# Performance work log

Measured on AMD Instinct MI355X. Metric: run time of the kernel, lower is better.

Reference implementation:

```python
import jax, jax.numpy as jnp
import numpy as np

INPUT_DIM = 2048
DIM = 1024
CODEBOOK_SIZE = 8192
COMMITMENT_COST = 0.25
N = 8192


def setup_inputs() -> dict:
    key = jax.random.key(0)
    ks = jax.random.split(key, 6)
    s_in = 1.0 / np.sqrt(INPUT_DIM)
    s_d = 1.0 / np.sqrt(DIM)
    return {
        "roi_feats": jax.random.normal(ks[0], (N, INPUT_DIM), dtype=jnp.float32),
        "W_in": jax.random.normal(ks[1], (DIM, INPUT_DIM), dtype=jnp.float32) * s_in,
        "b_in": jnp.zeros((DIM,), dtype=jnp.float32),
        "W_enc": jax.random.normal(ks[2], (DIM, DIM), dtype=jnp.float32) * s_d,
        "b_enc": jnp.zeros((DIM,), dtype=jnp.float32),
        "codebook": jax.random.uniform(ks[3], (CODEBOOK_SIZE, DIM), dtype=jnp.float32,
                                        minval=-1.0 / CODEBOOK_SIZE, maxval=1.0 / CODEBOOK_SIZE),
        "W_dec": jax.random.normal(ks[4], (DIM, DIM), dtype=jnp.float32) * s_d,
        "b_dec": jnp.zeros((DIM,), dtype=jnp.float32),
        "W_out": jax.random.normal(ks[5], (INPUT_DIM, DIM), dtype=jnp.float32) * s_d,
        "b_out": jnp.zeros((INPUT_DIM,), dtype=jnp.float32),
    }


def reference(roi_feats, W_in, b_in, W_enc, b_enc, codebook, W_dec, b_dec, W_out, b_out):
    # encoder(input_projection(x))
    z_e = (roi_feats @ W_in.T + b_in) @ W_enc.T + b_enc  # [N, DIM]
    # squared-euclidean distances to codebook: [N, K]
    d = (jnp.sum(z_e * z_e, axis=1, keepdims=True)
         - 2.0 * (z_e @ codebook.T)
         + jnp.sum(codebook * codebook, axis=1))
    ids = jnp.argmin(d, axis=-1)  # [N]
    z_q_raw = codebook[ids]  # [N, DIM]
    # straight-through estimator
    z_q = z_e + jax.lax.stop_gradient(z_q_raw - z_e)
    recon = (z_q @ W_dec.T + b_dec) @ W_out.T + b_out  # [N, INPUT_DIM]
    recon_loss = jnp.mean((recon - roi_feats) ** 2)
    embedding_loss = jnp.mean((jax.lax.stop_gradient(z_q) - z_e) ** 2)
    commitment_loss = jnp.mean((z_q - jax.lax.stop_gradient(z_e)) ** 2)
    vq_loss = recon_loss + embedding_loss + COMMITMENT_COST * commitment_loss
    return ids, z_q, recon, vq_loss, recon_loss, embedding_loss, commitment_loss
```

## Files before the change

### kernel.cpp

```cpp
#include <hip/hip_runtime.h>
#include <float.h>


#define N_ROWS 8192
#define IN_DIM 2048
#define DIM 1024
#define CBK 8192

#define PANEL_MASK_K1024_C32 0x0000000000401000ULL
#define PANEL_MASK_K2048_C32 0x0101001001001000ULL

#define SCREEN_DELTA 1.2e-3f

typedef __attribute__((ext_vector_type(8))) short short8;
typedef __attribute__((ext_vector_type(8))) unsigned short ushort8;
typedef __attribute__((ext_vector_type(4))) float f32x4;

__device__ __forceinline__ float sqf(float v) { return __builtin_fmaf(v, v, 0.0f); }

__device__ __forceinline__ unsigned short f2bf(float f) {
  unsigned int u = __float_as_uint(f);
  u += 0x7fffu + ((u >> 16) & 1u);
  return (unsigned short)(u >> 16);
}

__device__ __forceinline__ int swz128(int c) {
  return (c & 3) | (((c >> 3) & 7) << 2) | (((c >> 2) & 1) << 5) | ((c >> 6) << 6);
}

__device__ __forceinline__ float block_reduce_sum(float v) {
  __shared__ float sh[4];
  #pragma unroll
  for (int off = 32; off > 0; off >>= 1) v += __shfl_down(v, off, 64);
  const int lane = threadIdx.x & 63, w = threadIdx.x >> 6;
  if (lane == 0) sh[w] = v;
  __syncthreads();
  float r = 0.f;
  if (threadIdx.x == 0) r = sh[0] + sh[1] + sh[2] + sh[3];
  return r;
}

__device__ __forceinline__ float chain_d(const float* __restrict__ zsh,
                                         const float* __restrict__ cbr,
                                         float z2r, float c2e) {
  float part = 0.f;
  for (int k = 0; k < 384; ++k) part = __builtin_fmaf(zsh[k], cbr[k], part);
  float total = part;
  part = 0.f;
  for (int k = 384; k < 704; ++k) part = __builtin_fmaf(zsh[k], cbr[k], part);
  total = total + part;
  part = 0.f;
  for (int k = 704; k < 1024; ++k) part = __builtin_fmaf(zsh[k], cbr[k], part);
  total = total + part;
  return __builtin_fmaf(-2.0f, total, z2r) + c2e;
}

template <bool BT>
__global__ __launch_bounds__(256) void gemm128(
    const float* __restrict__ A, const float* __restrict__ B,
    const float* __restrict__ bias, float* __restrict__ C,
    int M, int N, int K) {
  __shared__ float As[2][16][132];
  __shared__ float Bs[2][16][132];
  const int tid = threadIdx.x;
  const int tx = tid & 15, ty = tid >> 4;
  const int bm = blockIdx.y, bn = blockIdx.x;

  const int mload = tid & 127, kh = tid >> 7;
  const size_t arow = (size_t)(bm * 128 + mload) * (size_t)K;
  const size_t brow = BT ? (size_t)(bn * 128 + mload) * (size_t)K : 0;
  const int swn = swz128(mload);
  const int c4 = (tid & 31) << 2;
  const int kr = tid >> 5;
  const int swc = swz128(c4);

  float acc[8][8];
  #pragma unroll
  for (int r = 0; r < 8; ++r)
    #pragma unroll
    for (int c = 0; c < 8; ++c) acc[r][c] = 0.f;

  const int boff = ((tx & 7) << 2) | ((tx >> 3) << 6);

  float4 av0, av1, bv0, bv1;
  av0 = *(const float4*)&A[arow + kh * 8];
  av1 = *(const float4*)&A[arow + kh * 8 + 4];
  if (BT) {
    bv0 = *(const float4*)&B[brow + kh * 8];
    bv1 = *(const float4*)&B[brow + kh * 8 + 4];
  } else {
    bv0 = *(const float4*)&B[(size_t)kr * N + bn * 128 + c4];
    bv1 = *(const float4*)&B[(size_t)(kr + 8) * N + bn * 128 + c4];
  }
  As[0][kh * 8 + 0][mload] = av0.x; As[0][kh * 8 + 1][mload] = av0.y;
  As[0][kh * 8 + 2][mload] = av0.z; As[0][kh * 8 + 3][mload] = av0.w;
  As[0][kh * 8 + 4][mload] = av1.x; As[0][kh * 8 + 5][mload] = av1.y;
  As[0][kh * 8 + 6][mload] = av1.z; As[0][kh * 8 + 7][mload] = av1.w;
  if (BT) {
    Bs[0][kh * 8 + 0][swn] = bv0.x; Bs[0][kh * 8 + 1][swn] = bv0.y;
    Bs[0][kh * 8 + 2][swn] = bv0.z; Bs[0][kh * 8 + 3][swn] = bv0.w;
    Bs[0][kh * 8 + 4][swn] = bv1.x; Bs[0][kh * 8 + 5][swn] = bv1.y;
    Bs[0][kh * 8 + 6][swn] = bv1.z; Bs[0][kh * 8 + 7][swn] = bv1.w;
  } else {
    *(float4*)&Bs[0][kr][swc] = bv0;
    *(float4*)&Bs[0][kr + 8][swc] = bv1;
  }
  const int nk = K >> 4;
  if (nk > 1) {
    av0 = *(const float4*)&A[arow + 16 + kh * 8];
    av1 = *(const float4*)&A[arow + 16 + kh * 8 + 4];
    if (BT) {
      bv0 = *(const float4*)&B[brow + 16 + kh * 8];
      bv1 = *(const float4*)&B[brow + 16 + kh * 8 + 4];
    } else {
      bv0 = *(const float4*)&B[(size_t)(16 + kr) * N + bn * 128 + c4];
      bv1 = *(const float4*)&B[(size_t)(16 + kr + 8) * N + bn * 128 + c4];
    }
  }
  __syncthreads();

  for (int ki = 0; ki < nk; ++ki) {
    const int p = ki & 1;
    if (ki + 1 < nk) {
      As[p ^ 1][kh * 8 + 0][mload] = av0.x; As[p ^ 1][kh * 8 + 1][mload] = av0.y;
      As[p ^ 1][kh * 8 + 2][mload] = av0.z; As[p ^ 1][kh * 8 + 3][mload] = av0.w;
      As[p ^ 1][kh * 8 + 4][mload] = av1.x; As[p ^ 1][kh * 8 + 5][mload] = av1.y;
      As[p ^ 1][kh * 8 + 6][mload] = av1.z; As[p ^ 1][kh * 8 + 7][mload] = av1.w;
      if (BT) {
        Bs[p ^ 1][kh * 8 + 0][swn] = bv0.x; Bs[p ^ 1][kh * 8 + 1][swn] = bv0.y;
        Bs[p ^ 1][kh * 8 + 2][swn] = bv0.z; Bs[p ^ 1][kh * 8 + 3][swn] = bv0.w;
        Bs[p ^ 1][kh * 8 + 4][swn] = bv1.x; Bs[p ^ 1][kh * 8 + 5][swn] = bv1.y;
        Bs[p ^ 1][kh * 8 + 6][swn] = bv1.z; Bs[p ^ 1][kh * 8 + 7][swn] = bv1.w;
      } else {
        *(float4*)&Bs[p ^ 1][kr][swc] = bv0;
        *(float4*)&Bs[p ^ 1][kr + 8][swc] = bv1;
      }
      if (ki + 2 < nk) {
        const int k2 = (ki + 2) << 4;
        av0 = *(const float4*)&A[arow + k2 + kh * 8];
        av1 = *(const float4*)&A[arow + k2 + kh * 8 + 4];
        if (BT) {
          bv0 = *(const float4*)&B[brow + k2 + kh * 8];
          bv1 = *(const float4*)&B[brow + k2 + kh * 8 + 4];
        } else {
          bv0 = *(const float4*)&B[(size_t)(k2 + kr) * N + bn * 128 + c4];
          bv1 = *(const float4*)&B[(size_t)(k2 + kr + 8) * N + bn * 128 + c4];
        }
      }
    }
    #pragma unroll
    for (int kk = 0; kk < 16; ++kk) {
      const float4 a0 = *(const float4*)&As[p][kk][ty * 8];
      const float4 a1 = *(const float4*)&As[p][kk][ty * 8 + 4];
      const float4 b0 = *(const float4*)&Bs[p][kk][boff];
      const float4 b1 = *(const float4*)&Bs[p][kk][boff + 32];
      const float ar[8] = {a0.x, a0.y, a0.z, a0.w, a1.x, a1.y, a1.z, a1.w};
      const float br[8] = {b0.x, b0.y, b0.z, b0.w, b1.x, b1.y, b1.z, b1.w};
      #pragma unroll
      for (int r = 0; r < 8; ++r)
        #pragma unroll
        for (int c = 0; c < 8; ++c) acc[r][c] = fmaf(ar[r], br[c], acc[r][c]);
    }
    __syncthreads();
  }

  const int gcol = bn * 128 + tx * 8;
  float bb[8] = {0, 0, 0, 0, 0, 0, 0, 0};
  if (bias) {
    const float4 v0 = *(const float4*)&bias[gcol];
    const float4 v1 = *(const float4*)&bias[gcol + 4];
    bb[0] = v0.x; bb[1] = v0.y; bb[2] = v0.z; bb[3] = v0.w;
    bb[4] = v1.x; bb[5] = v1.y; bb[6] = v1.z; bb[7] = v1.w;
  }
  #pragma unroll
  for (int r = 0; r < 8; ++r) {
    float* cp = &C[(size_t)(bm * 128 + ty * 8 + r) * N + gcol];
    float4 o0, o1;
    o0.x = acc[r][0] + bb[0]; o0.y = acc[r][1] + bb[1];
    o0.z = acc[r][2] + bb[2]; o0.w = acc[r][3] + bb[3];
    o1.x = acc[r][4] + bb[4]; o1.y = acc[r][5] + bb[5];
    o1.z = acc[r][6] + bb[6]; o1.w = acc[r][7] + bb[7];
    *(float4*)cp = o0;
    *(float4*)(cp + 4) = o1;
  }
}

__global__ __launch_bounds__(256) void emul_gemm_kernel(
    const float* __restrict__ A, const float* __restrict__ B,
    const float* __restrict__ bias, float* __restrict__ C,
    int N, int K, int lda, int ldb, unsigned long long panel_mask) {
  __shared__ float As_[2][32][128];
  __shared__ float Bs_[2][32][128];
  const int tid = threadIdx.x;
  const int tx = tid & 15, ty = tid >> 4;
  const int row0 = blockIdx.y * 128, col0 = blockIdx.x * 128;
  const int sr = tid & 127, sh = tid >> 7;
  const int scol = (((sr >> 2) & 1) << 6) + ((sr >> 3) << 2) + (sr & 3);

  float part[8][8], total[8][8];
  #pragma unroll
  for (int r = 0; r < 8; ++r)
    #pragma unroll
    for (int e = 0; e < 8; ++e) { part[r][e] = 0.f; total[r][e] = 0.f; }

  float4 av[4], bv[4];
  #pragma unroll
  for (int q = 0; q < 4; ++q) {
    av[q] = *(const float4*)&A[(size_t)(row0 + sr) * lda + sh * 16 + q * 4];
    bv[q] = *(const float4*)&B[(size_t)(col0 + sr) * ldb + sh * 16 + q * 4];
  }
  #pragma unroll
  for (int q = 0; q < 4; ++q) {
    As_[0][sh * 16 + q * 4 + 0][sr] = av[q].x;
    As_[0][sh * 16 + q * 4 + 1][sr] = av[q].y;
    As_[0][sh * 16 + q * 4 + 2][sr] = av[q].z;
    As_[0][sh * 16 + q * 4 + 3][sr] = av[q].w;
    Bs_[0][sh * 16 + q * 4 + 0][scol] = bv[q].x;
    Bs_[0][sh * 16 + q * 4 + 1][scol] = bv[q].y;
    Bs_[0][sh * 16 + q * 4 + 2][scol] = bv[q].z;
    Bs_[0][sh * 16 + q * 4 + 3][scol] = bv[q].w;
  }
  const int nch = K >> 5;
  if (nch > 1) {
    #pragma unroll
    for (int q = 0; q < 4; ++q) {
      av[q] = *(const float4*)&A[(size_t)(row0 + sr) * lda + 32 + sh * 16 + q * 4];
      bv[q] = *(const float4*)&B[(size_t)(col0 + sr) * ldb + 32 + sh * 16 + q * 4];
    }
  }
  __syncthreads();

  for (int ci = 0; ci < nch; ++ci) {
    const int p = ci & 1;
    if (ci + 1 < nch) {
      #pragma unroll
      for (int q = 0; q < 4; ++q) {
        As_[p ^ 1][sh * 16 + q * 4 + 0][sr] = av[q].x;
        As_[p ^ 1][sh * 16 + q * 4 + 1][sr] = av[q].y;
        As_[p ^ 1][sh * 16 + q * 4 + 2][sr] = av[q].z;
        As_[p ^ 1][sh * 16 + q * 4 + 3][sr] = av[q].w;
        Bs_[p ^ 1][sh * 16 + q * 4 + 0][scol] = bv[q].x;
        Bs_[p ^ 1][sh * 16 + q * 4 + 1][scol] = bv[q].y;
        Bs_[p ^ 1][sh * 16 + q * 4 + 2][scol] = bv[q].z;
        Bs_[p ^ 1][sh * 16 + q * 4 + 3][scol] = bv[q].w;
      }
      if (ci + 2 < nch) {
        const int k2 = (ci + 2) << 5;
        #pragma unroll
        for (int q = 0; q < 4; ++q) {
          av[q] = *(const float4*)&A[(size_t)(row0 + sr) * lda + k2 + sh * 16 + q * 4];
          bv[q] = *(const float4*)&B[(size_t)(col0 + sr) * ldb + k2 + sh * 16 + q * 4];
        }
      }
    }
    if (ci && ((panel_mask >> ci) & 1ULL)) {
      #pragma unroll
      for (int r = 0; r < 8; ++r)
        #pragma unroll
        for (int e = 0; e < 8; ++e) { total[r][e] = total[r][e] + part[r][e]; part[r][e] = 0.f; }
    }
    #pragma unroll 4
    for (int kk = 0; kk < 32; ++kk) {
      const float4 za = *(const float4*)&As_[p][kk][ty * 8];
      const float4 zb = *(const float4*)&As_[p][kk][ty * 8 + 4];
      const float4 ca = *(const float4*)&Bs_[p][kk][tx * 4];
      const float4 cb4 = *(const float4*)&Bs_[p][kk][64 + tx * 4];
      const float zr[8] = {za.x, za.y, za.z, za.w, zb.x, zb.y, zb.z, zb.w};
      const float cr[8] = {ca.x, ca.y, ca.z, ca.w, cb4.x, cb4.y, cb4.z, cb4.w};
      #pragma unroll
      for (int r = 0; r < 8; ++r)
        #pragma unroll
        for (int e = 0; e < 8; ++e)
          part[r][e] = __builtin_fmaf(zr[r], cr[e], part[r][e]);
    }
    __syncthreads();
  }
  #pragma unroll
  for (int r = 0; r < 8; ++r)
    #pragma unroll
    for (int e = 0; e < 8; ++e) total[r][e] = total[r][e] + part[r][e];

  const float4 ba = *(const float4*)&bias[col0 + tx * 8];
  const float4 bb = *(const float4*)&bias[col0 + tx * 8 + 4];
  const float br8[8] = {ba.x, ba.y, ba.z, ba.w, bb.x, bb.y, bb.z, bb.w};
  #pragma unroll
  for (int r = 0; r < 8; ++r) {
    float* cp = &C[(size_t)(row0 + ty * 8 + r) * N + col0 + tx * 8];
    float4 o0, o1;
    o0.x = total[r][0] + br8[0]; o0.y = total[r][1] + br8[1];
    o0.z = total[r][2] + br8[2]; o0.w = total[r][3] + br8[3];
    o1.x = total[r][4] + br8[4]; o1.y = total[r][5] + br8[5];
    o1.z = total[r][6] + br8[6]; o1.w = total[r][7] + br8[7];
    *(float4*)cp = o0;
    *(float4*)(cp + 4) = o1;
  }
}

__global__ __launch_bounds__(256) void zsplit_kernel(
    const float* __restrict__ Z, unsigned* __restrict__ ZP) {
  const size_t base = (size_t)blockIdx.x * 1024 + threadIdx.x * 4;
  const float4 v = *(const float4*)&Z[base];
  const float xf[4] = {v.x, v.y, v.z, v.w};
  uint4 o;
  unsigned ov[4];
  #pragma unroll
  for (int i = 0; i < 4; ++i) {
    const unsigned u = __float_as_uint(xf[i]);
    const unsigned hb = u & 0xFFFF0000u;
    const float rem = xf[i] - __uint_as_float(hb);
    ov[i] = (u >> 16) | (__float_as_uint(rem) & 0xFFFF0000u);
  }
  o.x = ov[0]; o.y = ov[1]; o.z = ov[2]; o.w = ov[3];
  *(uint4*)&ZP[base] = o;
}

__global__ __launch_bounds__(256) void mfma_screen_kernel(
    const unsigned* __restrict__ ZP, const float* __restrict__ CB,
    const float* __restrict__ Z2, const float* __restrict__ C2,
    uint4* __restrict__ recs) {
  __shared__ unsigned short Zs[128 * 64];
  __shared__ unsigned short Cs[128 * 64];
  __shared__ int rowminI[128];
  __shared__ int cnt[128];
  __shared__ unsigned short cand[128][12];
  const int tid = threadIdx.x;
  const int wid = tid >> 6, lane = tid & 63;
  const int e0 = blockIdx.x * 128, row0 = blockIdx.y * 128;
  const int wr = (wid >> 1) * 64, wc = (wid & 1) * 64;

  if (tid < 128) { rowminI[tid] = 0x7F800000; cnt[tid] = 0; }

  f32x4 acc[4][4];
  #pragma unroll
  for (int m = 0; m < 4; ++m)
    #pragma unroll
    for (int n = 0; n < 4; ++n)
      #pragma unroll
      for (int j = 0; j < 4; ++j) acc[m][n][j] = 0.f;

  const int stg_r = tid >> 3, stg_kg = (tid & 7) * 4;

  for (int k0 = 0; k0 < 1024; k0 += 32) {
    __syncthreads();
    #pragma unroll
    for (int s = 0; s < 4; ++s) {
      const int r = stg_r + s * 32;
      const int swz = (r & 7) << 4;
      const int bhi = (r * 128 + stg_kg * 2) ^ swz;
      const int blo = (r * 128 + 64 + stg_kg * 2) ^ swz;
      const uint4 p = *(const uint4*)&ZP[(size_t)(row0 + r) * 1024 + k0 + stg_kg];
      uint2 zh, zl;
      zh.x = (p.x & 0xFFFFu) | (p.y << 16);
      zh.y = (p.z & 0xFFFFu) | (p.w << 16);
      zl.x = (p.x >> 16) | (p.y & 0xFFFF0000u);
      zl.y = (p.z >> 16) | (p.w & 0xFFFF0000u);
      *(uint2*)((char*)Zs + bhi) = zh;
      *(uint2*)((char*)Zs + blo) = zl;
      const float4 cv = *(const float4*)&CB[(size_t)(e0 + r) * 1024 + k0 + stg_kg];
      const float cf[4] = {cv.x, cv.y, cv.z, cv.w};
      unsigned ch[4], cl[4];
      #pragma unroll
      for (int i = 0; i < 4; ++i) {
        const unsigned u = __float_as_uint(cf[i]);
        ch[i] = u & 0xFFFF0000u;
        const float rem = cf[i] - __uint_as_float(ch[i]);
        cl[i] = __float_as_uint(rem) & 0xFFFF0000u;
      }
      uint2 cph, cpl;
      cph.x = (ch[0] >> 16) | ch[1];
      cph.y = (ch[2] >> 16) | ch[3];
      cpl.x = (cl[0] >> 16) | cl[1];
      cpl.y = (cl[2] >> 16) | cl[3];
      *(uint2*)((char*)Cs + bhi) = cph;
      *(uint2*)((char*)Cs + blo) = cpl;
    }
    __syncthreads();
    const int kb2 = 16 * (lane >> 4);
    short8 ah[4], al[4], bh[4], bl[4];
    #pragma unroll
    for (int m = 0; m < 4; ++m) {
      const int r = wr + m * 16 + (lane & 15);
      const int swz = (r & 7) << 4;
      ah[m] = *(const short8*)((const char*)Zs + ((r * 128 + kb2) ^ swz));
      al[m] = *(const short8*)((const char*)Zs + ((r * 128 + 64 + kb2) ^ swz));
    }
    #pragma unroll
    for (int n = 0; n < 4; ++n) {
      const int r = wc + n * 16 + (lane & 15);
      const int swz = (r & 7) << 4;
      bh[n] = *(const short8*)((const char*)Cs + ((r * 128 + kb2) ^ swz));
      bl[n] = *(const short8*)((const char*)Cs + ((r * 128 + 64 + kb2) ^ swz));
    }
    #pragma unroll
    for (int m = 0; m < 4; ++m)
      #pragma unroll
      for (int n = 0; n < 4; ++n) {
        acc[m][n] = __builtin_amdgcn_mfma_f32_16x16x32_bf16(ah[m], bh[n], acc[m][n], 0, 0, 0);
        acc[m][n] = __builtin_amdgcn_mfma_f32_16x16x32_bf16(ah[m], bl[n], acc[m][n], 0, 0, 0);
        acc[m][n] = __builtin_amdgcn_mfma_f32_16x16x32_bf16(al[m], bh[n], acc[m][n], 0, 0, 0);
      }
  }

  float dv[4][4][4];
  #pragma unroll
  for (int m = 0; m < 4; ++m)
    #pragma unroll
    for (int j = 0; j < 4; ++j) {
      const int rg = row0 + wr + m * 16 + (lane >> 4) * 4 + j;
      const float z2r = Z2[rg];
      float lm = FLT_MAX;
      #pragma unroll
      for (int n = 0; n < 4; ++n) {
        const float d = __builtin_fmaf(-2.0f, acc[m][n][j], z2r) +
                        C2[e0 + wc + n * 16 + (lane & 15)];
        dv[m][n][j] = d;
        lm = fminf(lm, d);
      }
      atomicMin(&rowminI[wr + m * 16 + (lane >> 4) * 4 + j], __float_as_int(lm));
    }
  __syncthreads();
  #pragma unroll
  for (int m = 0; m < 4; ++m)
    #pragma unroll
    for (int j = 0; j < 4; ++j) {
      const int rl = wr + m * 16 + (lane >> 4) * 4 + j;
      const float thr = __int_as_float(rowminI[rl]) + SCREEN_DELTA;
      #pragma unroll
      for (int n = 0; n < 4; ++n) {
        if (dv[m][n][j] <= thr) {
          const int pos = atomicAdd(&cnt[rl], 1);
          if (pos < 12)
            cand[rl][pos] = (unsigned short)(e0 + wc + n * 16 + (lane & 15));
        }
      }
    }
  __syncthreads();
  if (tid < 128) {
    uint4 a, b;
    a.x = (unsigned)rowminI[tid];
    a.y = (unsigned)cnt[tid];
    a.z = (unsigned)cand[tid][0] | ((unsigned)cand[tid][1] << 16);
    a.w = (unsigned)cand[tid][2] | ((unsigned)cand[tid][3] << 16);
    b.x = (unsigned)cand[tid][4] | ((unsigned)cand[tid][5] << 16);
    b.y = (unsigned)cand[tid][6] | ((unsigned)cand[tid][7] << 16);
    b.z = (unsigned)cand[tid][8] | ((unsigned)cand[tid][9] << 16);
    b.w = (unsigned)cand[tid][10] | ((unsigned)cand[tid][11] << 16);
    const size_t base = ((size_t)(row0 + tid) * 64 + blockIdx.x) * 2;
    recs[base] = a;
    recs[base + 1] = b;
  }
}

__global__ __launch_bounds__(256) void collect_rescore_kernel(
    const uint4* __restrict__ recs, const float* __restrict__ Z,
    const float* __restrict__ CB, const float* __restrict__ Z2,
    const float* __restrict__ C2, int* __restrict__ ids,
    float* __restrict__ o_ids) {
  __shared__ float zsh[1024];
  __shared__ float gmin_sh;
  __shared__ int lcnt, ovf;
  __shared__ unsigned short list[64];
  __shared__ unsigned long long kred[4];
  const int row = blockIdx.x, tid = threadIdx.x;
  if (tid == 0) { lcnt = 0; ovf = 0; }
  uint4 r0 = make_uint4(0, 0, 0, 0), r1 = make_uint4(0, 0, 0, 0);
  float mymin = FLT_MAX;
  if (tid < 64) {
    const size_t base = ((size_t)row * 64 + tid) * 2;
    r0 = recs[base];
    r1 = recs[base + 1];
    mymin = __uint_as_float(r0.x);
  }
  for (int i = tid; i < 1024; i += 256) zsh[i] = Z[(size_t)row * 1024 + i];
  if (tid < 64) {
    float m = mymin;
    #pragma unroll
    for (int off = 32; off > 0; off >>= 1) m = fminf(m, __shfl_down(m, off, 64));
    if (tid == 0) gmin_sh = m;
  }
  __syncthreads();
  const float thr = gmin_sh + SCREEN_DELTA;
  if (tid < 64 && mymin <= thr) {
    const int c = (int)r0.y;
    if (c > 12) {
      atomicOr(&ovf, 1);
    } else {
      unsigned short idxs[12];
      idxs[0] = r0.z & 0xFFFF; idxs[1] = r0.z >> 16;
      idxs[2] = r0.w & 0xFFFF; idxs[3] = r0.w >> 16;
      idxs[4] = r1.x & 0xFFFF; idxs[5] = r1.x >> 16;
      idxs[6] = r1.y & 0xFFFF; idxs[7] = r1.y >> 16;
      idxs[8] = r1.z & 0xFFFF; idxs[9] = r1.z >> 16;
      idxs[10] = r1.w & 0xFFFF; idxs[11] = r1.w >> 16;
      for (int i = 0; i < c; ++i) {
        const int pos = atomicAdd(&lcnt, 1);
        if (pos < 64) list[pos] = idxs[i];
        else atomicOr(&ovf, 1);
      }
    }
  }
  __syncthreads();
  const float z2r = Z2[row];
  unsigned long long key = ~0ULL;
  if (ovf) {
    for (int e = tid; e < CBK; e += 256) {
      const float d = chain_d(zsh, &CB[(size_t)e * 1024], z2r, C2[e]);
      const unsigned long long k =
          ((unsigned long long)__float_as_uint(d) << 32) | (unsigned)e;
      key = (k < key) ? k : key;
    }
  } else {
    const int n = lcnt < 64 ? lcnt : 64;
    if (tid < n) {
      const int e = list[tid];
      const float d = chain_d(zsh, &CB[(size_t)e * 1024], z2r, C2[e]);
      key = ((unsigned long long)__float_as_uint(d) << 32) | (unsigned)e;
    }
  }
  #pragma unroll
  for (int off = 32; off > 0; off >>= 1) {
    const unsigned long long o = __shfl_down(key, off, 64);
    key = (o < key) ? o : key;
  }
  if ((tid & 63) == 0) kred[tid >> 6] = key;
  __syncthreads();
  if (tid == 0) {
    unsigned long long k = kred[0];
    k = (kred[1] < k) ? kred[1] : k;
    k = (kred[2] < k) ? kred[2] : k;
    k = (kred[3] < k) ? kred[3] : k;
    const int e = (int)(k & 0xFFFFFFFFu);
    ids[row] = e;
    o_ids[row] = (float)e;
  }
}

__global__ __launch_bounds__(256) void mfma_recon_kernel(
    const float* __restrict__ A, const float* __restrict__ B,
    const float* __restrict__ bias, float* __restrict__ C) {
  __shared__ unsigned short Abf[128 * 64];
  __shared__ unsigned short Bbf[128 * 64];
  const int tid = threadIdx.x;
  const int wid = tid >> 6, lane = tid & 63;
  const int row0 = blockIdx.y * 128, col0 = blockIdx.x * 128;
  const int wr = (wid >> 1) * 64, wc = (wid & 1) * 64;

  f32x4 acc[4][4];
  #pragma unroll
  for (int m = 0; m < 4; ++m)
    #pragma unroll
    for (int n = 0; n < 4; ++n)
      #pragma unroll
      for (int j = 0; j < 4; ++j) acc[m][n][j] = 0.f;

  for (int k0 = 0; k0 < 1024; k0 += 64) {
    __syncthreads();
    #pragma unroll
    for (int q = 0; q < 4; ++q) {
      const int g = tid + q * 256;
      const int r = g >> 3;
      const int kg = (g & 7) * 8;
      const float4 a0 = *(const float4*)&A[(size_t)(row0 + r) * 1024 + k0 + kg];
      const float4 a1 = *(const float4*)&A[(size_t)(row0 + r) * 1024 + k0 + kg + 4];
      const float4 b0 = *(const float4*)&B[(size_t)(col0 + r) * 1024 + k0 + kg];
      const float4 b1 = *(const float4*)&B[(size_t)(col0 + r) * 1024 + k0 + kg + 4];
      ushort8 pa, pb;
      pa[0] = f2bf(a0.x); pa[1] = f2bf(a0.y); pa[2] = f2bf(a0.z); pa[3] = f2bf(a0.w);
      pa[4] = f2bf(a1.x); pa[5] = f2bf(a1.y); pa[6] = f2bf(a1.z); pa[7] = f2bf(a1.w);
      pb[0] = f2bf(b0.x); pb[1] = f2bf(b0.y); pb[2] = f2bf(b0.z); pb[3] = f2bf(b0.w);
      pb[4] = f2bf(b1.x); pb[5] = f2bf(b1.y); pb[6] = f2bf(b1.z); pb[7] = f2bf(b1.w);
      const int byte = (r * 128 + kg * 2) ^ ((r & 7) << 4);
      *(ushort8*)((char*)Abf + byte) = pa;
      *(ushort8*)((char*)Bbf + byte) = pb;
    }
    __syncthreads();
    #pragma unroll
    for (int kh = 0; kh < 2; ++kh) {
      const int kb = kh * 32 + 8 * (lane >> 4);
      short8 afr[4], bfr[4];
      #pragma unroll
      for (int m = 0; m < 4; ++m) {
        const int r = wr + m * 16 + (lane & 15);
        const int byte = (r * 128 + kb * 2) ^ ((r & 7) << 4);
        afr[m] = *(const short8*)((const char*)Abf + byte);
      }
      #pragma unroll
      for (int n = 0; n < 4; ++n) {
        const int r = wc + n * 16 + (lane & 15);
        const int byte = (r * 128 + kb * 2) ^ ((r & 7) << 4);
        bfr[n] = *(const short8*)((const char*)Bbf + byte);
      }
      #pragma unroll
      for (int m = 0; m < 4; ++m)
        #pragma unroll
        for (int n = 0; n < 4; ++n)
          acc[m][n] = __builtin_amdgcn_mfma_f32_16x16x32_bf16(
              afr[m], bfr[n], acc[m][n], 0, 0, 0);
    }
  }

  #pragma unroll
  for (int m = 0; m < 4; ++m)
    #pragma unroll
    for (int n = 0; n < 4; ++n) {
      const int col = col0 + wc + n * 16 + (lane & 15);
      const float bc = bias[col];
      #pragma unroll
      for (int j = 0; j < 4; ++j) {
        const int row = row0 + wr + m * 16 + (lane >> 4) * 4 + j;
        C[(size_t)row * 2048 + col] = acc[m][n][j] + bc;
      }
    }
}

__global__ __launch_bounds__(256) void sumsq1024_kernel(
    const float* __restrict__ X, float* __restrict__ out) {
  __shared__ float rows[4][1024];
  __shared__ float leaves[4][8];
  const int tid = threadIdx.x;
  const int row0 = blockIdx.x * 4;
  for (int i = tid; i < 4096; i += 256)
    rows[i >> 10][i & 1023] = X[(size_t)row0 * 1024 + i];
  __syncthreads();
  if (tid < 32) {
    const int r = tid >> 3, lf = tid & 7;
    const float* a = &rows[r][lf * 128];
    float s0 = sqf(a[0]), s1 = sqf(a[1]), s2 = sqf(a[2]), s3 = sqf(a[3]);
    float s4 = sqf(a[4]), s5 = sqf(a[5]), s6 = sqf(a[6]), s7 = sqf(a[7]);
    for (int i = 8; i < 128; i += 8) {
      s0 = s0 + sqf(a[i + 0]); s1 = s1 + sqf(a[i + 1]);
      s2 = s2 + sqf(a[i + 2]); s3 = s3 + sqf(a[i + 3]);
      s4 = s4 + sqf(a[i + 4]); s5 = s5 + sqf(a[i + 5]);
      s6 = s6 + sqf(a[i + 6]); s7 = s7 + sqf(a[i + 7]);
    }
    leaves[r][lf] = ((s0 + s1) + (s2 + s3)) + ((s4 + s5) + (s6 + s7));
  }
  __syncthreads();
  if (tid < 4) {
    const float* L = leaves[tid];
    const float p01 = L[0] + L[1], p23 = L[2] + L[3];
    const float p45 = L[4] + L[5], p67 = L[6] + L[7];
    out[row0 + tid] = ((p01 + p23) + (p45 + p67));
  }
}

__global__ __launch_bounds__(256) void gather_zq_kernel(
    const float* __restrict__ cb, const int* __restrict__ ids,
    float* __restrict__ zq) {
  const int row = blockIdx.x;
  const int id = ids[row];
  const float4 v = *(const float4*)&cb[(size_t)id * DIM + threadIdx.x * 4];
  *(float4*)&zq[(size_t)row * DIM + threadIdx.x * 4] = v;
}

__global__ __launch_bounds__(256) void rowdot_bias_kernel(
    const float* __restrict__ W, const float* __restrict__ v,
    const float* __restrict__ b2, float* __restrict__ out) {
  const int row = blockIdx.x;
  const float4 w4 = *(const float4*)&W[(size_t)row * 1024 + threadIdx.x * 4];
  const float4 v4 = *(const float4*)&v[threadIdx.x * 4];
  const float s = w4.x * v4.x + w4.y * v4.y + w4.z * v4.z + w4.w * v4.w;
  const float r = block_reduce_sum(s);
  if (threadIdx.x == 0) out[row] = r + b2[row];
}

__global__ __launch_bounds__(256) void sqdiff_partial_kernel(
    const float* __restrict__ a, const float* __restrict__ b,
    float* __restrict__ part) {
  const size_t base = (size_t)blockIdx.x * 2048 + (size_t)threadIdx.x * 8;
  const float4 x0 = *(const float4*)&a[base];
  const float4 x1 = *(const float4*)&a[base + 4];
  const float4 y0 = *(const float4*)&b[base];
  const float4 y1 = *(const float4*)&b[base + 4];
  float s = 0.f;
  float d;
  d = x0.x - y0.x; s += d * d; d = x0.y - y0.y; s += d * d;
  d = x0.z - y0.z; s += d * d; d = x0.w - y0.w; s += d * d;
  d = x1.x - y1.x; s += d * d; d = x1.y - y1.y; s += d * d;
  d = x1.z - y1.z; s += d * d; d = x1.w - y1.w; s += d * d;
  const float r = block_reduce_sum(s);
  if (threadIdx.x == 0) part[blockIdx.x] = r;
}

__global__ __launch_bounds__(256) void final_losses_kernel(
    const float* __restrict__ rp, const float* __restrict__ ep,
    float* __restrict__ o) {
  __shared__ double sh[4];
  const int lane = threadIdx.x & 63, w = threadIdx.x >> 6;
  double s = 0.0;
  for (int i = threadIdx.x; i < 8192; i += 256) s += (double)rp[i];
  #pragma unroll
  for (int off = 32; off > 0; off >>= 1) s += __shfl_down(s, off, 64);
  if (lane == 0) sh[w] = s;
  __syncthreads();
  double rl = 0.0;
  if (threadIdx.x == 0) rl = (sh[0] + sh[1] + sh[2] + sh[3]) / ((double)N_ROWS * IN_DIM);
  __syncthreads();
  double s2 = 0.0;
  for (int i = threadIdx.x; i < 4096; i += 256) s2 += (double)ep[i];
  #pragma unroll
  for (int off = 32; off > 0; off >>= 1) s2 += __shfl_down(s2, off, 64);
  if (lane == 0) sh[w] = s2;
  __syncthreads();
  if (threadIdx.x == 0) {
    const double el = (sh[0] + sh[1] + sh[2] + sh[3]) / ((double)N_ROWS * DIM);
    o[0] = (float)(rl + el + 0.25 * el);
    o[1] = (float)rl;
    o[2] = (float)el;
    o[3] = (float)el;
  }
}

extern "C" void kernel_launch(void* const* d_in, const int* in_sizes, int n_in,
                              void* d_out, int out_size, void* d_ws, size_t ws_size,
                              hipStream_t stream) {
  const float* roi   = (const float*)d_in[0];
  const float* W_in  = (const float*)d_in[1];
  const float* b_in  = (const float*)d_in[2];
  const float* W_enc = (const float*)d_in[3];
  const float* b_enc = (const float*)d_in[4];
  const float* cb    = (const float*)d_in[5];
  const float* W_dec = (const float*)d_in[6];
  const float* b_dec = (const float*)d_in[7];
  const float* W_out = (const float*)d_in[8];
  const float* b_out = (const float*)d_in[9];

  float* out = (float*)d_out;
  float* o_ids   = out;
  float* o_zq    = out + 8192;
  float* o_recon = out + 8192 + (size_t)N_ROWS * DIM;
  float* o_scal  = out + 8192 + (size_t)N_ROWS * DIM + (size_t)N_ROWS * IN_DIM;

  float*  ws    = (float*)d_ws;
  float*  W_dc  = ws;
  float*  z2    = ws + 2097152;
  float*  c2    = ws + 2105344;
  int*    ids   = (int*)(ws + 2113536);
  float*  b_dc  = ws + 2121728;
  float*  ep    = ws + 2123776;
  float*  rp    = ws + 2127872;

  float*    t     = o_recon;
  float*    z     = o_recon + (size_t)N_ROWS * DIM;
  unsigned* zpack = (unsigned*)o_recon;
  uint4*    recs  = (uint4*)o_zq;

  rowdot_bias_kernel<<<IN_DIM, 256, 0, stream>>>(W_out, b_dec, b_out, b_dc);
  gemm128<false><<<dim3(DIM / 128, IN_DIM / 128), 256, 0, stream>>>(
      W_out, W_dec, nullptr, W_dc, IN_DIM, DIM, DIM);

  emul_gemm_kernel<<<dim3(DIM / 128, N_ROWS / 128), 256, 0, stream>>>(
      roi, W_in, b_in, t, DIM, IN_DIM, IN_DIM, IN_DIM, PANEL_MASK_K2048_C32);
  emul_gemm_kernel<<<dim3(DIM / 128, N_ROWS / 128), 256, 0, stream>>>(
      t, W_enc, b_enc, z, DIM, DIM, DIM, DIM, PANEL_MASK_K1024_C32);

  sumsq1024_kernel<<<N_ROWS / 4, 256, 0, stream>>>(z, z2);
  sumsq1024_kernel<<<CBK / 4, 256, 0, stream>>>(cb, c2);

  zsplit_kernel<<<N_ROWS, 256, 0, stream>>>(z, zpack);

  mfma_screen_kernel<<<dim3(CBK / 128, N_ROWS / 128), 256, 0, stream>>>(
      zpack, cb, z2, c2, recs);
  collect_rescore_kernel<<<N_ROWS, 256, 0, stream>>>(
      recs, z, cb, z2, c2, ids, o_ids);

  gather_zq_kernel<<<N_ROWS, 256, 0, stream>>>(cb, ids, o_zq);
  sqdiff_partial_kernel<<<(N_ROWS * DIM) / 2048, 256, 0, stream>>>(o_zq, z, ep);

  mfma_recon_kernel<<<dim3(IN_DIM / 128, N_ROWS / 128), 256, 0, stream>>>(
      o_zq, W_dc, b_dc, o_recon);

  sqdiff_partial_kernel<<<(N_ROWS * IN_DIM) / 2048, 256, 0, stream>>>(
      o_recon, roi, rp);
  final_losses_kernel<<<1, 256, 0, stream>>>(rp, ep, o_scal);
}
```

Baseline: 1.486 ms.

## Fuse z split, zq gather and embedding loss; widen screen K tile

The bf16 hi/lo split of z moves into the epilogue of the second encoder GEMM, and the codebook gather plus per-row embedding-loss sum move into the rescoring kernel. This removes the separate zsplit, gather and sqdiff kernels and their extra passes over memory. The screening kernel now stages 64 K-elements per iteration with twice the shared memory, halving barrier count. Its row-min atomics are reduced across 16 lanes by shuffles first. Workspace aliasing of recs and zpack is swapped between the output buffers, and the larger LDS footprint may lower occupancy.

```diff
diff --git a/kernel.cpp b/kernel.cpp
--- a/kernel.cpp
+++ b/kernel.cpp
@@ -22,6 +22,13 @@
   unsigned int u = __float_as_uint(f);
   u += 0x7fffu + ((u >> 16) & 1u);
   return (unsigned short)(u >> 16);
+}
+
+__device__ __forceinline__ unsigned packsplit(float x) {
+  const unsigned u = __float_as_uint(x);
+  const unsigned hb = u & 0xFFFF0000u;
+  const float rem = x - __uint_as_float(hb);
+  return (u >> 16) | (__float_as_uint(rem) & 0xFFFF0000u);
 }
 
 __device__ __forceinline__ int swz128(int c) {
@@ -188,6 +195,7 @@
 __global__ __launch_bounds__(256) void emul_gemm_kernel(
     const float* __restrict__ A, const float* __restrict__ B,
     const float* __restrict__ bias, float* __restrict__ C,
+    unsigned* __restrict__ ZP,
     int N, int K, int lda, int ldb, unsigned long long panel_mask) {
   __shared__ float As_[2][32][128];
   __shared__ float Bs_[2][32][128];
@@ -285,41 +293,35 @@
   const float br8[8] = {ba.x, ba.y, ba.z, ba.w, bb.x, bb.y, bb.z, bb.w};
   #pragma unroll
   for (int r = 0; r < 8; ++r) {
-    float* cp = &C[(size_t)(row0 + ty * 8 + r) * N + col0 + tx * 8];
+    const size_t rowi = (size_t)(row0 + ty * 8 + r);
+    float ov[8];
+    #pragma unroll
+    for (int j = 0; j < 8; ++j) ov[j] = total[r][j] + br8[j];
+    float* cp = &C[rowi * N + col0 + tx * 8];
     float4 o0, o1;
-    o0.x = total[r][0] + br8[0]; o0.y = total[r][1] + br8[1];
-    o0.z = total[r][2] + br8[2]; o0.w = total[r][3] + br8[3];
-    o1.x = total[r][4] + br8[4]; o1.y = total[r][5] + br8[5];
-    o1.z = total[r][6] + br8[6]; o1.w = total[r][7] + br8[7];
+    o0.x = ov[0]; o0.y = ov[1]; o0.z = ov[2]; o0.w = ov[3];
+    o1.x = ov[4]; o1.y = ov[5]; o1.z = ov[6]; o1.w = ov[7];
     *(float4*)cp = o0;
     *(float4*)(cp + 4) = o1;
-  }
-}
-
-__global__ __launch_bounds__(256) void zsplit_kernel(
-    const float* __restrict__ Z, unsigned* __restrict__ ZP) {
-  const size_t base = (size_t)blockIdx.x * 1024 + threadIdx.x * 4;
-  const float4 v = *(const float4*)&Z[base];
-  const float xf[4] = {v.x, v.y, v.z, v.w};
-  uint4 o;
-  unsigned ov[4];
-  #pragma unroll
-  for (int i = 0; i < 4; ++i) {
-    const unsigned u = __float_as_uint(xf[i]);
-    const unsigned hb = u & 0xFFFF0000u;
-    const float rem = xf[i] - __uint_as_float(hb);
-    ov[i] = (u >> 16) | (__float_as_uint(rem) & 0xFFFF0000u);
-  }
-  o.x = ov[0]; o.y = ov[1]; o.z = ov[2]; o.w = ov[3];
-  *(uint4*)&ZP[base] = o;
+    if (ZP) {
+      uint4 p0, p1;
+      p0.x = packsplit(ov[0]); p0.y = packsplit(ov[1]);
+      p0.z = packsplit(ov[2]); p0.w = packsplit(ov[3]);
+      p1.x = packsplit(ov[4]); p1.y = packsplit(ov[5]);
+      p1.z = packsplit(ov[6]); p1.w = packsplit(ov[7]);
+      unsigned* zp = &ZP[rowi * N + col0 + tx * 8];
+      *(uint4*)zp = p0;
+      *(uint4*)(zp + 4) = p1;
+    }
+  }
 }
 
 __global__ __launch_bounds__(256) void mfma_screen_kernel(
     const unsigned* __restrict__ ZP, const float* __restrict__ CB,
     const float* __restrict__ Z2, const float* __restrict__ C2,
     uint4* __restrict__ recs) {
-  __shared__ unsigned short Zs[128 * 64];
-  __shared__ unsigned short Cs[128 * 64];
+  __shared__ unsigned short Zs[128 * 128];
+  __shared__ unsigned short Cs[128 * 128];
   __shared__ int rowminI[128];
   __shared__ int cnt[128];
   __shared__ unsigned short cand[128][12];
@@ -338,17 +340,18 @@
       #pragma unroll
       for (int j = 0; j < 4; ++j) acc[m][n][j] = 0.f;
 
-  const int stg_r = tid >> 3, stg_kg = (tid & 7) * 4;
-
-  for (int k0 = 0; k0 < 1024; k0 += 32) {
+  const int stg_r = tid >> 4;
+  const int stg_k4 = (tid & 15) * 4;
+
+  for (int k0 = 0; k0 < 1024; k0 += 64) {
     __syncthreads();
     #pragma unroll
-    for (int s = 0; s < 4; ++s) {
-      const int r = stg_r + s * 32;
+    for (int s = 0; s < 8; ++s) {
+      const int r = stg_r + s * 16;
       const int swz = (r & 7) << 4;
-      const int bhi = (r * 128 + stg_kg * 2) ^ swz;
-      const int blo = (r * 128 + 64 + stg_kg * 2) ^ swz;
-      const uint4 p = *(const uint4*)&ZP[(size_t)(row0 + r) * 1024 + k0 + stg_kg];
+      const int bhi = (r * 256 + stg_k4 * 2) ^ swz;
+      const int blo = (r * 256 + 128 + stg_k4 * 2) ^ swz;
+      const uint4 p = *(const uint4*)&ZP[(size_t)(row0 + r) * 1024 + k0 + stg_k4];
       uint2 zh, zl;
       zh.x = (p.x & 0xFFFFu) | (p.y << 16);
       zh.y = (p.z & 0xFFFFu) | (p.w << 16);
@@ -356,7 +359,7 @@
       zl.y = (p.z >> 16) | (p.w & 0xFFFF0000u);
       *(uint2*)((char*)Zs + bhi) = zh;
       *(uint2*)((char*)Zs + blo) = zl;
-      const float4 cv = *(const float4*)&CB[(size_t)(e0 + r) * 1024 + k0 + stg_kg];
+      const float4 cv = *(const float4*)&CB[(size_t)(e0 + r) * 1024 + k0 + stg_k4];
       const float cf[4] = {cv.x, cv.y, cv.z, cv.w};
       unsigned ch[4], cl[4];
       #pragma unroll
@@ -375,30 +378,33 @@
       *(uint2*)((char*)Cs + blo) = cpl;
     }
     __syncthreads();
-    const int kb2 = 16 * (lane >> 4);
-    short8 ah[4], al[4], bh[4], bl[4];
-    #pragma unroll
-    for (int m = 0; m < 4; ++m) {
-      const int r = wr + m * 16 + (lane & 15);
-      const int swz = (r & 7) << 4;
-      ah[m] = *(const short8*)((const char*)Zs + ((r * 128 + kb2) ^ swz));
-      al[m] = *(const short8*)((const char*)Zs + ((r * 128 + 64 + kb2) ^ swz));
-    }
-    #pragma unroll
-    for (int n = 0; n < 4; ++n) {
-      const int r = wc + n * 16 + (lane & 15);
-      const int swz = (r & 7) << 4;
-      bh[n] = *(const short8*)((const char*)Cs + ((r * 128 + kb2) ^ swz));
-      bl[n] = *(const short8*)((const char*)Cs + ((r * 128 + 64 + kb2) ^ swz));
-    }
-    #pragma unroll
-    for (int m = 0; m < 4; ++m)
+    #pragma unroll
+    for (int kh = 0; kh < 2; ++kh) {
+      const int kb = kh * 64 + 16 * (lane >> 4);
+      short8 ah[4], al[4], bh[4], bl[4];
+      #pragma unroll
+      for (int m = 0; m < 4; ++m) {
+        const int r = wr + m * 16 + (lane & 15);
+        const int swz = (r & 7) << 4;
+        ah[m] = *(const short8*)((const char*)Zs + ((r * 256 + kb) ^ swz));
+        al[m] = *(const short8*)((const char*)Zs + ((r * 256 + 128 + kb) ^ swz));
+      }
       #pragma unroll
       for (int n = 0; n < 4; ++n) {
-        acc[m][n] = __builtin_amdgcn_mfma_f32_16x16x32_bf16(ah[m], bh[n], acc[m][n], 0, 0, 0);
-        acc[m][n] = __builtin_amdgcn_mfma_f32_16x16x32_bf16(ah[m], bl[n], acc[m][n], 0, 0, 0);
-        acc[m][n] = __builtin_amdgcn_mfma_f32_16x16x32_bf16(al[m], bh[n], acc[m][n], 0, 0, 0);
-      }
+        const int r = wc + n * 16 + (lane & 15);
+        const int swz = (r & 7) << 4;
+        bh[n] = *(const short8*)((const char*)Cs + ((r * 256 + kb) ^ swz));
+        bl[n] = *(const short8*)((const char*)Cs + ((r * 256 + 128 + kb) ^ swz));
+      }
+      #pragma unroll
+      for (int m = 0; m < 4; ++m)
+        #pragma unroll
+        for (int n = 0; n < 4; ++n) {
+          acc[m][n] = __builtin_amdgcn_mfma_f32_16x16x32_bf16(ah[m], bh[n], acc[m][n], 0, 0, 0);
+          acc[m][n] = __builtin_amdgcn_mfma_f32_16x16x32_bf16(ah[m], bl[n], acc[m][n], 0, 0, 0);
+          acc[m][n] = __builtin_amdgcn_mfma_f32_16x16x32_bf16(al[m], bh[n], acc[m][n], 0, 0, 0);
+        }
+    }
   }
 
   float dv[4][4][4];
@@ -416,7 +422,11 @@
         dv[m][n][j] = d;
         lm = fminf(lm, d);
       }
-      atomicMin(&rowminI[wr + m * 16 + (lane >> 4) * 4 + j], __float_as_int(lm));
+      #pragma unroll
+      for (int msk = 1; msk < 16; msk <<= 1)
+        lm = fminf(lm, __shfl_xor(lm, msk, 64));
+      if ((lane & 15) == 0)
+        atomicMin(&rowminI[wr + m * 16 + (lane >> 4) * 4 + j], __float_as_int(lm));
     }
   __syncthreads();
   #pragma unroll
@@ -455,10 +465,11 @@
     const uint4* __restrict__ recs, const float* __restrict__ Z,
     const float* __restrict__ CB, const float* __restrict__ Z2,
     const float* __restrict__ C2, int* __restrict__ ids,
-    float* __restrict__ o_ids) {
+    float* __restrict__ o_ids, float* __restrict__ o_zq,
+    float* __restrict__ esum) {
   __shared__ float zsh[1024];
   __shared__ float gmin_sh;
-  __shared__ int lcnt, ovf;
+  __shared__ int lcnt, ovf, ewin;
   __shared__ unsigned short list[64];
   __shared__ unsigned long long kred[4];
   const int row = blockIdx.x, tid = threadIdx.x;
@@ -532,7 +543,19 @@
     const int e = (int)(k & 0xFFFFFFFFu);
     ids[row] = e;
     o_ids[row] = (float)e;
-  }
+    ewin = e;
+  }
+  __syncthreads();
+  const int e2 = ewin;
+  float s = 0.f;
+  for (int i = tid; i < 1024; i += 256) {
+    const float c = CB[(size_t)e2 * 1024 + i];
+    o_zq[(size_t)row * 1024 + i] = c;
+    const float d = zsh[i] - c;
+    s = __builtin_fmaf(d, d, s);
+  }
+  const float r2 = block_reduce_sum(s);
+  if (tid == 0) esum[row] = r2;
 }
 
 __global__ __launch_bounds__(256) void mfma_recon_kernel(
@@ -644,15 +667,6 @@
   }
 }
 
-__global__ __launch_bounds__(256) void gather_zq_kernel(
-    const float* __restrict__ cb, const int* __restrict__ ids,
-    float* __restrict__ zq) {
-  const int row = blockIdx.x;
-  const int id = ids[row];
-  const float4 v = *(const float4*)&cb[(size_t)id * DIM + threadIdx.x * 4];
-  *(float4*)&zq[(size_t)row * DIM + threadIdx.x * 4] = v;
-}
-
 __global__ __launch_bounds__(256) void rowdot_bias_kernel(
     const float* __restrict__ W, const float* __restrict__ v,
     const float* __restrict__ b2, float* __restrict__ out) {
@@ -683,7 +697,7 @@
 }
 
 __global__ __launch_bounds__(256) void final_losses_kernel(
-    const float* __restrict__ rp, const float* __restrict__ ep,
+    const float* __restrict__ rp, const float* __restrict__ esum,
     float* __restrict__ o) {
   __shared__ double sh[4];
   const int lane = threadIdx.x & 63, w = threadIdx.x >> 6;
@@ -697,7 +711,7 @@
   if (threadIdx.x == 0) rl = (sh[0] + sh[1] + sh[2] + sh[3]) / ((double)N_ROWS * IN_DIM);
   __syncthreads();
   double s2 = 0.0;
-  for (int i = threadIdx.x; i < 4096; i += 256) s2 += (double)ep[i];
+  for (int i = threadIdx.x; i < 8192; i += 256) s2 += (double)esum[i];
   #pragma unroll
   for (int off = 32; off > 0; off >>= 1) s2 += __shfl_down(s2, off, 64);
   if (lane == 0) sh[w] = s2;
@@ -737,40 +751,36 @@
   float*  c2    = ws + 2105344;
   int*    ids   = (int*)(ws + 2113536);
   float*  b_dc  = ws + 2121728;
-  float*  ep    = ws + 2123776;
-  float*  rp    = ws + 2127872;
+  float*  esum  = ws + 2123776;
+  float*  rp    = ws + 2131968;
 
   float*    t     = o_recon;
   float*    z     = o_recon + (size_t)N_ROWS * DIM;
-  unsigned* zpack = (unsigned*)o_recon;
-  uint4*    recs  = (uint4*)o_zq;
+  uint4*    recs  = (uint4*)o_recon;
+  unsigned* zpack = (unsigned*)o_zq;
 
   rowdot_bias_kernel<<<IN_DIM, 256, 0, stream>>>(W_out, b_dec, b_out, b_dc);
   gemm128<false><<<dim3(DIM / 128, IN_DIM / 128), 256, 0, stream>>>(
       W_out, W_dec, nullptr, W_dc, IN_DIM, DIM, DIM);
 
   emul_gemm_kernel<<<dim3(DIM / 128, N_ROWS / 128), 256, 0, stream>>>(
-      roi, W_in, b_in, t, DIM, IN_DIM, IN_DIM, IN_DIM, PANEL_MASK_K2048_C32);
+      roi, W_in, b_in, t, nullptr, DIM, IN_DIM, IN_DIM, IN_DIM,
+      PANEL_MASK_K2048_C32);
   emul_gemm_kernel<<<dim3(DIM / 128, N_ROWS / 128), 256, 0, stream>>>(
-      t, W_enc, b_enc, z, DIM, DIM, DIM, DIM, PANEL_MASK_K1024_C32);
+      t, W_enc, b_enc, z, zpack, DIM, DIM, DIM, DIM, PANEL_MASK_K1024_C32);
 
   sumsq1024_kernel<<<N_ROWS / 4, 256, 0, stream>>>(z, z2);
   sumsq1024_kernel<<<CBK / 4, 256, 0, stream>>>(cb, c2);
-
-  zsplit_kernel<<<N_ROWS, 256, 0, stream>>>(z, zpack);
 
   mfma_screen_kernel<<<dim3(CBK / 128, N_ROWS / 128), 256, 0, stream>>>(
       zpack, cb, z2, c2, recs);
   collect_rescore_kernel<<<N_ROWS, 256, 0, stream>>>(
-      recs, z, cb, z2, c2, ids, o_ids);
-
-  gather_zq_kernel<<<N_ROWS, 256, 0, stream>>>(cb, ids, o_zq);
-  sqdiff_partial_kernel<<<(N_ROWS * DIM) / 2048, 256, 0, stream>>>(o_zq, z, ep);
+      recs, z, cb, z2, c2, ids, o_ids, o_zq, esum);
 
   mfma_recon_kernel<<<dim3(IN_DIM / 128, N_ROWS / 128), 256, 0, stream>>>(
       o_zq, W_dc, b_dc, o_recon);
 
   sqdiff_partial_kernel<<<(N_ROWS * IN_DIM) / 2048, 256, 0, stream>>>(
       o_recon, roi, rp);
-  final_losses_kernel<<<1, 256, 0, stream>>>(rp, ep, o_scal);
-}
+  final_losses_kernel<<<1, 256, 0, stream>>>(rp, esum, o_scal);
+}
```

Measured after the change: 1.861 ms. 25.3% more time.
